# Kernel tuning notes

Hardware: AMD Instinct MI355X
Metric: run time of the kernel (lower is better)

## Reference

```python
import jax, jax.numpy as jnp
import numpy as np

N_PAPER = 100000
N_AUTHOR = 50000
E = 800000
D_IN, D_HID, D_OUT = 128, 128, 64


def seg_max(x, src, dst, num_segments):
    # adj_t.matmul(x, reduce='max'): per-destination max over neighbor features;
    # destinations with no in-edges get 0 (torch_sparse convention).
    m = jax.ops.segment_max(x[src], dst, num_segments=num_segments)
    return jnp.where(jnp.isneginf(m), jnp.zeros((), m.dtype), m)


def setup_inputs() -> dict:
    key = jax.random.key(0)
    ks = jax.random.split(key, 32)
    inp = {}
    inp['x_paper'] = jax.random.normal(ks[0], (N_PAPER, D_IN), jnp.float32)
    inp['emb_author'] = jax.random.normal(ks[1], (N_AUTHOR, D_IN), jnp.float32)
    inp['writes_src'] = jax.random.randint(ks[2], (E,), 0, N_AUTHOR, jnp.int32)
    inp['writes_dst'] = jax.random.randint(ks[3], (E,), 0, N_PAPER, jnp.int32)
    inp['cites_src'] = jax.random.randint(ks[4], (E,), 0, N_PAPER, jnp.int32)
    inp['cites_dst'] = jax.random.randint(ks[5], (E,), 0, N_PAPER, jnp.int32)
    inp['wb_src'] = jax.random.randint(ks[6], (E,), 0, N_PAPER, jnp.int32)
    inp['wb_dst'] = jax.random.randint(ks[7], (E,), 0, N_AUTHOR, jnp.int32)

    def lin_w(k, din, dout):
        s = 1.0 / np.sqrt(din)
        return jax.random.uniform(k, (din, dout), jnp.float32, -s, s)

    # layer 1: D_IN -> D_HID
    inp['w1_rel_writes'] = lin_w(ks[8], D_IN, D_HID)
    inp['w1_rel_cites'] = lin_w(ks[9], D_IN, D_HID)
    inp['w1_rel_wb'] = lin_w(ks[10], D_IN, D_HID)
    inp['w1_root_paper'] = lin_w(ks[11], D_IN, D_HID)
    inp['b1_root_paper'] = jnp.zeros((D_HID,), jnp.float32)
    inp['w1_root_author'] = lin_w(ks[12], D_IN, D_HID)
    inp['b1_root_author'] = jnp.zeros((D_HID,), jnp.float32)
    # layer 2: D_HID -> D_OUT
    inp['w2_rel_writes'] = lin_w(ks[13], D_HID, D_OUT)
    inp['w2_rel_cites'] = lin_w(ks[14], D_HID, D_OUT)
    inp['w2_rel_wb'] = lin_w(ks[15], D_HID, D_OUT)
    inp['w2_root_paper'] = lin_w(ks[16], D_HID, D_OUT)
    inp['b2_root_paper'] = jnp.zeros((D_OUT,), jnp.float32)
    inp['w2_root_author'] = lin_w(ks[17], D_HID, D_OUT)
    inp['b2_root_author'] = jnp.zeros((D_OUT,), jnp.float32)
    return inp


def _conv(xp, xa, edges, w_writes, w_cites, w_wb, w_rp, b_rp, w_ra, b_ra):
    writes_src, writes_dst, cites_src, cites_dst, wb_src, wb_dst = edges
    out_p = xp @ w_rp + b_rp
    out_a = xa @ w_ra + b_ra
    out_p = out_p + seg_max(xa, writes_src, writes_dst, N_PAPER) @ w_writes
    out_p = out_p + seg_max(xp, cites_src, cites_dst, N_PAPER) @ w_cites
    out_a = out_a + seg_max(xp, wb_src, wb_dst, N_AUTHOR) @ w_wb
    return out_p, out_a


def reference(x_paper, emb_author,
              writes_src, writes_dst, cites_src, cites_dst, wb_src, wb_dst,
              w1_rel_writes, w1_rel_cites, w1_rel_wb,
              w1_root_paper, b1_root_paper, w1_root_author, b1_root_author,
              w2_rel_writes, w2_rel_cites, w2_rel_wb,
              w2_root_paper, b2_root_paper, w2_root_author, b2_root_author):
    edges = (writes_src, writes_dst, cites_src, cites_dst, wb_src, wb_dst)
    hp, ha = _conv(x_paper, emb_author, edges,
                   w1_rel_writes, w1_rel_cites, w1_rel_wb,
                   w1_root_paper, b1_root_paper, w1_root_author, b1_root_author)
    hp, ha = jax.nn.relu(hp), jax.nn.relu(ha)  # dropout p=0 -> identity
    return _conv(hp, ha, edges,
                 w2_rel_writes, w2_rel_cites, w2_rel_wb,
                 w2_root_paper, b2_root_paper, w2_root_author, b2_root_author)
```

## Files before the change

kernel.cpp:

```cpp
#include <hip/hip_runtime.h>


#define DI 128
#define NP 100000
#define NA 50000
#define EPB 4096
#define MAXBIN 391

typedef short s8v __attribute__((ext_vector_type(8)));
typedef float f32x4 __attribute__((ext_vector_type(4)));

__device__ __forceinline__ unsigned short bf16_rne(float f) {
  unsigned int fb = __float_as_uint(f);
  fb += 0x7FFFu + ((fb >> 16) & 1u);
  return (unsigned short)(fb >> 16);
}

struct R3Args {
  const int* src[3]; const int* dst[3];
  int* bh[3]; int* bhs[3];
  unsigned int* tmp[3];
  int* bkt[3]; int* cnt[3]; int* rs[3];
  int E[3]; int N[3]; int nbin[3]; int NB[3];
};

__global__ __launch_bounds__(256) void radix_s1_k(R3Args a) {
  int y = blockIdx.y, blk = blockIdx.x;
  int NB = a.NB[y];
  if (blk >= NB) return;
  __shared__ int hist[MAXBIN];
  int nbin = a.nbin[y];
  for (int i = threadIdx.x; i < nbin; i += 256) hist[i] = 0;
  __syncthreads();
  int e0 = blk * EPB, e1 = min(e0 + EPB, a.E[y]);
  const int* dst = a.dst[y];
  for (int e = e0 + threadIdx.x; e < e1; e += 256)
    atomicAdd(&hist[dst[e] >> 8], 1);
  __syncthreads();
  int* bh = a.bh[y];
  for (int i = threadIdx.x; i < nbin; i += 256) bh[i * NB + blk] = hist[i];
}

__global__ __launch_bounds__(256) void radix_x1_k(R3Args a) {
  int y = blockIdx.y, blk = blockIdx.x;
  int NB = a.NB[y];
  if (blk >= NB) return;
  __shared__ int cur[MAXBIN];
  int nbin = a.nbin[y];
  const int* bhs = a.bhs[y];
  for (int i = threadIdx.x; i < nbin; i += 256) cur[i] = bhs[i * NB + blk];
  __syncthreads();
  int e0 = blk * EPB, e1 = min(e0 + EPB, a.E[y]);
  const int* dst = a.dst[y];
  const int* src = a.src[y];
  unsigned int* tmp = a.tmp[y];
  for (int e = e0 + threadIdx.x; e < e1; e += 256) {
    int d = dst[e];
    int pos = atomicAdd(&cur[d >> 8], 1);
    tmp[pos] = ((unsigned int)(d & 255) << 24) | (unsigned int)src[e];
  }
}

struct WArgs {
  const float* w[10];
  unsigned short* wf[10];
};

struct P2CArgs {
  R3Args ra;
  WArgs wa;
  const float* Xp; unsigned short* Yp; int n4p;
  const float* Xa; unsigned short* Ya; int n4a;
  int p2Blocks;
  int maxbin;
};

__global__ __launch_bounds__(256) void p2cvt_k(P2CArgs a) {
  int bid = blockIdx.x;
  int t = threadIdx.x;
  if (bid < a.p2Blocks) {
    int y = bid / a.maxbin, bin = bid % a.maxbin;
    if (bin >= a.ra.nbin[y]) return;
    __shared__ int hist[256], scn[256], cursor[256];
    hist[t] = 0;
    __syncthreads();
    const int* bhs = a.ra.bhs[y];
    int NB = a.ra.NB[y];
    int base = bhs[bin * NB];
    int end  = (bin + 1 < a.ra.nbin[y]) ? bhs[(bin + 1) * NB] : a.ra.E[y];
    const unsigned int* tmp = a.ra.tmp[y];
    for (int i = base + t; i < end; i += 256)
      atomicAdd(&hist[tmp[i] >> 24], 1);
    __syncthreads();
    int v = hist[t];
    scn[t] = v; __syncthreads();
    int acc = v;
    for (int o = 1; o < 256; o <<= 1) {
      int u = (t >= o) ? scn[t - o] : 0;
      __syncthreads();
      acc += u; scn[t] = acc;
      __syncthreads();
    }
    int ex = acc - v;
    cursor[t] = ex;
    int d = bin * 256 + t;
    if (d < a.ra.N[y]) { a.ra.cnt[y][d] = v; a.ra.rs[y][d] = base + ex; }
    __syncthreads();
    int* bkt = a.ra.bkt[y];
    for (int i = base + t; i < end; i += 256) {
      unsigned int p = tmp[i];
      int pos = atomicAdd(&cursor[p >> 24], 1);
      bkt[base + pos] = (int)((p & 0xFFFFFFu) << 8);
    }
    return;
  }
  bid -= a.p2Blocks;
  if (bid < 80) {
    int widx = bid >> 3;
    int OUTi = (widx < 5) ? 128 : 64;
    int CF = OUTi / 16;
    int nt = 4 * CF * 64;
    int tg = (bid & 7) * 256 + t;
    if (tg >= nt) return;
    int lane = tg & 63, tmp2 = tg >> 6;
    int cf = tmp2 % CF, kc = tmp2 / CF;
    int k0 = kc * 32 + (lane >> 4) * 8;
    int c  = cf * 16 + (lane & 15);
    const float* w = a.wa.w[widx];
    s8v v;
    #pragma unroll
    for (int i = 0; i < 8; ++i) v[i] = (short)bf16_rne(w[(k0 + i) * OUTi + c]);
    *(reinterpret_cast<s8v*>(a.wa.wf[widx]) + tg) = v;
    return;
  }
  bid -= 80;
  int i = bid * 256 + t;
  const float* X; unsigned short* Y;
  if (i < a.n4p) { X = a.Xp; Y = a.Yp; }
  else { i -= a.n4p; if (i >= a.n4a) return; X = a.Xa; Y = a.Ya; }
  float4 f = reinterpret_cast<const float4*>(X)[i];
  ushort4 o;
  o.x = bf16_rne(f.x); o.y = bf16_rne(f.y); o.z = bf16_rne(f.z); o.w = bf16_rne(f.w);
  reinterpret_cast<ushort4*>(Y)[i] = o;
}

struct S3Args {
  const int* cnt[3]; int* bsum[3]; int* rs[3];
  int n[3]; int nb[3];
};

__global__ __launch_bounds__(256) void blocksum3_k(S3Args a) {
  int y = blockIdx.y;
  int n = a.n[y];
  if (blockIdx.x * 1024 >= n) return;
  __shared__ int red[256];
  int t = threadIdx.x;
  int base = blockIdx.x * 1024 + t * 4;
  int s = 0;
  #pragma unroll
  for (int i = 0; i < 4; ++i) { int idx = base + i; if (idx < n) s += a.cnt[y][idx]; }
  red[t] = s; __syncthreads();
  #pragma unroll
  for (int o = 128; o > 0; o >>= 1) { if (t < o) red[t] += red[t + o]; __syncthreads(); }
  if (t == 0) a.bsum[y][blockIdx.x] = red[0];
}

__global__ __launch_bounds__(256) void partials3_k(S3Args a) {
  __shared__ int sm[256];
  int y = blockIdx.x;
  int nb = a.nb[y];
  int t = threadIdx.x;
  int v = (t < nb) ? a.bsum[y][t] : 0;
  sm[t] = v; __syncthreads();
  int acc = v;
  for (int o = 1; o < 256; o <<= 1) {
    int u = (t >= o) ? sm[t - o] : 0;
    __syncthreads();
    acc += u; sm[t] = acc;
    __syncthreads();
  }
  if (t < nb) a.bsum[y][t] = acc - v;
}

__global__ __launch_bounds__(256) void scanwrite3_k(S3Args a) {
  int y = blockIdx.y;
  int n = a.n[y];
  if (blockIdx.x * 1024 >= n) return;
  __shared__ int ts[256];
  int t = threadIdx.x;
  int base = blockIdx.x * 1024 + t * 4;
  int v[4]; int s = 0;
  #pragma unroll
  for (int i = 0; i < 4; ++i) { int idx = base + i; v[i] = (idx < n) ? a.cnt[y][idx] : 0; s += v[i]; }
  ts[t] = s; __syncthreads();
  int inc = s;
  for (int o = 1; o < 256; o <<= 1) {
    int u = (t >= o) ? ts[t - o] : 0;
    __syncthreads();
    inc += u; ts[t] = inc;
    __syncthreads();
  }
  int p = a.bsum[y][blockIdx.x] + inc - s;
  #pragma unroll
  for (int i = 0; i < 4; ++i) { int idx = base + i; if (idx < n) { a.rs[y][idx] = p; p += v[i]; } }
}

struct G3Args {
  const int* cnt[3]; const int* rs[3]; const int* bkt[3];
  const unsigned short* X[3]; unsigned short* S[3];
  int N[3];
};

__global__ __launch_bounds__(256) void gather3_k(G3Args a) {
  const int y = blockIdx.y;
  const int lane = threadIdx.x & 63;
  const int wave = threadIdx.x >> 6;
  const int g = lane >> 4, lg = lane & 15;
  const int d = blockIdx.x * 16 + wave * 4 + g;
  if (d >= a.N[y]) return;

  unsigned short* So = a.S[y] + (size_t)d * DI + lg * 8;
  const int deg = a.cnt[y][d];
  if (deg == 0) {
    uint4 z; z.x = z.y = z.z = z.w = 0u;
    *reinterpret_cast<uint4*>(So) = z;
    return;
  }
  const int* bp = a.bkt[y] + a.rs[y][d];
  const char* Xb = reinterpret_cast<const char*>(a.X[y]) + lg * 16;

  float ml[4], mh[4];
  #pragma unroll
  for (int j = 0; j < 4; ++j) { ml[j] = -3.4e38f; mh[j] = -3.4e38f; }

  int s0 = bp[0];
  for (int e = 0; e < deg; e += 4) {
    int s1 = (e + 1 < deg) ? bp[e + 1] : s0;
    int s2 = (e + 2 < deg) ? bp[e + 2] : s0;
    int s3 = (e + 3 < deg) ? bp[e + 3] : s0;
    int sn = (e + 4 < deg) ? bp[e + 4] : s0;
    uint4 r0 = *reinterpret_cast<const uint4*>(Xb + s0);
    uint4 r1 = *reinterpret_cast<const uint4*>(Xb + s1);
    uint4 r2 = *reinterpret_cast<const uint4*>(Xb + s2);
    uint4 r3 = *reinterpret_cast<const uint4*>(Xb + s3);
    unsigned int w0[4] = {r0.x, r0.y, r0.z, r0.w};
    unsigned int w1[4] = {r1.x, r1.y, r1.z, r1.w};
    unsigned int w2[4] = {r2.x, r2.y, r2.z, r2.w};
    unsigned int w3[4] = {r3.x, r3.y, r3.z, r3.w};
    #pragma unroll
    for (int j = 0; j < 4; ++j) {
      float tl = fmaxf(fmaxf(__uint_as_float(w0[j] << 16), __uint_as_float(w1[j] << 16)),
                       __uint_as_float(w2[j] << 16));
      ml[j] = fmaxf(fmaxf(ml[j], __uint_as_float(w3[j] << 16)), tl);
      float th = fmaxf(fmaxf(__uint_as_float(w0[j]), __uint_as_float(w1[j])),
                       __uint_as_float(w2[j]));
      mh[j] = fmaxf(fmaxf(mh[j], __uint_as_float(w3[j])), th);
    }
    s0 = sn;
  }
  uint4 o;
  o.x = (__float_as_uint(ml[0]) >> 16) | (__float_as_uint(mh[0]) & 0xFFFF0000u);
  o.y = (__float_as_uint(ml[1]) >> 16) | (__float_as_uint(mh[1]) & 0xFFFF0000u);
  o.z = (__float_as_uint(ml[2]) >> 16) | (__float_as_uint(mh[2]) & 0xFFFF0000u);
  o.w = (__float_as_uint(ml[3]) >> 16) | (__float_as_uint(mh[3]) & 0xFFFF0000u);
  *reinterpret_cast<uint4*>(So) = o;
}

template<int CF>
__device__ __forceinline__ void mfma_accum(const unsigned short* __restrict__ A,
                                           const unsigned short* __restrict__ W,
                                           f32x4* acc, size_t arow, int lane, int half) {
  const s8v* a = reinterpret_cast<const s8v*>(A + arow * DI + half * 8);
  const s8v* w = reinterpret_cast<const s8v*>(W) + lane;
  #pragma unroll
  for (int kc = 0; kc < 4; ++kc) {
    s8v av = a[kc * 4];
    #pragma unroll
    for (int cf = 0; cf < CF; ++cf)
      acc[cf] = __builtin_amdgcn_mfma_f32_16x16x32_bf16(av, w[(kc * CF + cf) * 64], acc[cf], 0, 0, 0);
  }
}

struct GemmPairArgs {
  const unsigned short *A0[2], *W0[2], *A1[2], *W1[2], *A2, *W2;
  const float* bias[2];
  void* out[2];
  int N[2];
  int blocks0;
};

template<int OUT, bool RELU, bool OUT_BF16>
__global__ __launch_bounds__(256) void gemm_pair_k(GemmPairArgs g) {
  constexpr int CF = OUT / 16;
  const int p = (blockIdx.x >= (unsigned)g.blocks0) ? 1 : 0;
  const int brow = blockIdx.x - (p ? g.blocks0 : 0);
  const int N = g.N[p];
  const int lane = threadIdx.x & 63;
  const int wave = threadIdx.x >> 6;
  const int row0 = brow * 64 + wave * 16;
  if (row0 >= N) return;
  const int rl = lane & 15, half = lane >> 4;
  const size_t arow = (size_t)(row0 + rl);

  f32x4 acc[CF];
  #pragma unroll
  for (int i = 0; i < CF; ++i) acc[i] = f32x4{0.f, 0.f, 0.f, 0.f};

  mfma_accum<CF>(g.A0[p], g.W0[p], acc, arow, lane, half);
  mfma_accum<CF>(g.A1[p], g.W1[p], acc, arow, lane, half);
  if (!p) mfma_accum<CF>(g.A2, g.W2, acc, arow, lane, half);

  const float* bias = g.bias[p];
  #pragma unroll
  for (int cf = 0; cf < CF; ++cf) {
    float bv = bias[cf * 16 + rl];
    #pragma unroll
    for (int j = 0; j < 4; ++j) {
      int r = row0 + half * 4 + j;
      if (r >= N) continue;
      float v = acc[cf][j] + bv;
      if (RELU) v = v > 0.f ? v : 0.f;
      size_t idx = (size_t)r * OUT + cf * 16 + rl;
      if (OUT_BF16) ((unsigned short*)g.out[p])[idx] = bf16_rne(v);
      else          __builtin_nontemporal_store(v, (float*)g.out[p] + idx);
    }
  }
}

extern "C" void kernel_launch(void* const* d_in, const int* in_sizes, int n_in,
                              void* d_out, int out_size, void* d_ws, size_t ws_size,
                              hipStream_t stream) {
  const float* xp = (const float*)d_in[0];
  const float* xa = (const float*)d_in[1];
  const int* wsrc = (const int*)d_in[2];
  const int* wdst = (const int*)d_in[3];
  const int* csrc = (const int*)d_in[4];
  const int* cdst = (const int*)d_in[5];
  const int* bsrc = (const int*)d_in[6];
  const int* bdst = (const int*)d_in[7];
  const int Ew = in_sizes[2], Ec = in_sizes[4], Eb = in_sizes[6];

  const float* w1w  = (const float*)d_in[8];
  const float* w1c  = (const float*)d_in[9];
  const float* w1wb = (const float*)d_in[10];
  const float* w1rp = (const float*)d_in[11];
  const float* b1rp = (const float*)d_in[12];
  const float* w1ra = (const float*)d_in[13];
  const float* b1ra = (const float*)d_in[14];
  const float* w2w  = (const float*)d_in[15];
  const float* w2c  = (const float*)d_in[16];
  const float* w2wb = (const float*)d_in[17];
  const float* w2rp = (const float*)d_in[18];
  const float* b2rp = (const float*)d_in[19];
  const float* w2ra = (const float*)d_in[20];
  const float* b2ra = (const float*)d_in[21];

  char* ws = (char*)d_ws;
  unsigned short* xpb = (unsigned short*)(ws + 0);
  unsigned short* xab = (unsigned short*)(ws + 25600000);
  unsigned short* hp  = (unsigned short*)(ws + 38400000);
  unsigned short* ha  = (unsigned short*)(ws + 64000000);
  unsigned short* S_w = (unsigned short*)(ws + 76800000);
  unsigned short* S_c = (unsigned short*)(ws + 102400000);
  unsigned short* S_b = (unsigned short*)(ws + 128000000);
  int* bkt_w = (int*)(ws + 140800000);
  int* bkt_c = (int*)(ws + 144000000);
  int* bkt_b = (int*)(ws + 147200000);
  int* cnt_w = (int*)(ws + 150400000);
  int* cnt_c = (int*)(ws + 150800000);
  int* cnt_b = (int*)(ws + 151200000);
  int* rs_w  = (int*)(ws + 151400000);
  int* rs_c  = (int*)(ws + 151800000);
  int* rs_b  = (int*)(ws + 152200000);
  int* bsum_w = (int*)(ws + 152400000);
  int* bsum_c = (int*)(ws + 152404096);
  int* bsum_b = (int*)(ws + 152408192);
  unsigned short* wf = (unsigned short*)(ws + 152412288);
  unsigned int* tmp_w = (unsigned int*)(ws + 152660000);
  unsigned int* tmp_c = (unsigned int*)(ws + 155860000);
  unsigned int* tmp_b = (unsigned int*)(ws + 159060000);
  int* bh_w  = (int*)(ws + 76800000);
  int* bh_c  = (int*)(ws + 77110000);
  int* bh_b  = (int*)(ws + 77420000);
  int* bhs_w = (int*)(ws + 77580000);
  int* bhs_c = (int*)(ws + 77890000);
  int* bhs_b = (int*)(ws + 78200000);

  unsigned short* WF[10];
  size_t off = 0;
  for (int i = 0; i < 10; ++i) {
    WF[i] = wf + off;
    off += (i < 5) ? (size_t)128 * 128 : (size_t)128 * 64;
  }

  float* outP = (float*)d_out;
  float* outA = outP + (size_t)NP * 64;

  const int gP = (NP + 63) / 64, gA = (NA + 63) / 64;
  const int gG = (NP + 15) / 16;

  R3Args ra;
  ra.src[0] = wsrc; ra.dst[0] = wdst; ra.E[0] = Ew; ra.N[0] = NP;
  ra.src[1] = csrc; ra.dst[1] = cdst; ra.E[1] = Ec; ra.N[1] = NP;
  ra.src[2] = bsrc; ra.dst[2] = bdst; ra.E[2] = Eb; ra.N[2] = NA;
  ra.bh[0] = bh_w; ra.bh[1] = bh_c; ra.bh[2] = bh_b;
  ra.bhs[0] = bhs_w; ra.bhs[1] = bhs_c; ra.bhs[2] = bhs_b;
  ra.tmp[0] = tmp_w; ra.tmp[1] = tmp_c; ra.tmp[2] = tmp_b;
  ra.bkt[0] = bkt_w; ra.bkt[1] = bkt_c; ra.bkt[2] = bkt_b;
  ra.cnt[0] = cnt_w; ra.cnt[1] = cnt_c; ra.cnt[2] = cnt_b;
  ra.rs[0] = rs_w; ra.rs[1] = rs_c; ra.rs[2] = rs_b;
  int gSX = 0, gSC = 0, maxbin = 0;
  for (int y = 0; y < 3; ++y) {
    ra.nbin[y] = (ra.N[y] + 255) >> 8;
    ra.NB[y] = (ra.E[y] + EPB - 1) / EPB;
    if (ra.NB[y] > gSX) gSX = ra.NB[y];
    if (ra.nbin[y] > maxbin) maxbin = ra.nbin[y];
  }
  S3Args sa;
  sa.bsum[0] = bsum_w; sa.bsum[1] = bsum_c; sa.bsum[2] = bsum_b;
  for (int y = 0; y < 3; ++y) {
    sa.cnt[y] = ra.bh[y]; sa.rs[y] = ra.bhs[y];
    sa.n[y] = ra.nbin[y] * ra.NB[y];
    sa.nb[y] = (sa.n[y] + 1023) / 1024;
    if (sa.nb[y] > gSC) gSC = sa.nb[y];
  }

  const int n4p = NP * DI / 4, n4a = NA * DI / 4;
  P2CArgs pc;
  pc.ra = ra;
  const float* wsrcs[10] = {w1w, w1c, w1wb, w1rp, w1ra, w2w, w2c, w2wb, w2rp, w2ra};
  for (int i = 0; i < 10; ++i) { pc.wa.w[i] = wsrcs[i]; pc.wa.wf[i] = WF[i]; }
  pc.Xp = xp; pc.Yp = xpb; pc.n4p = n4p;
  pc.Xa = xa; pc.Ya = xab; pc.n4a = n4a;
  pc.maxbin = maxbin;
  pc.p2Blocks = 3 * maxbin;
  const int gPC = pc.p2Blocks + 80 + (n4p + n4a + 255) / 256;

  G3Args g1, g2;
  for (int i = 0; i < 3; ++i) {
    g1.cnt[i] = g2.cnt[i] = (i == 0) ? cnt_w : (i == 1) ? cnt_c : cnt_b;
    g1.rs[i]  = g2.rs[i]  = (i == 0) ? rs_w  : (i == 1) ? rs_c  : rs_b;
    g1.bkt[i] = g2.bkt[i] = (i == 0) ? bkt_w : (i == 1) ? bkt_c : bkt_b;
    g1.S[i]   = g2.S[i]   = (i == 0) ? S_w   : (i == 1) ? S_c   : S_b;
    g1.N[i]   = g2.N[i]   = (i == 2) ? NA : NP;
  }
  g1.X[0] = xab; g1.X[1] = xpb; g1.X[2] = xpb;
  g2.X[0] = ha;  g2.X[1] = hp;  g2.X[2] = hp;

  GemmPairArgs p1, p2;
  p1.A0[0] = xpb; p1.W0[0] = WF[3]; p1.A1[0] = S_w; p1.W1[0] = WF[0]; p1.A2 = S_c; p1.W2 = WF[1];
  p1.bias[0] = b1rp; p1.out[0] = hp; p1.N[0] = NP;
  p1.A0[1] = xab; p1.W0[1] = WF[4]; p1.A1[1] = S_b; p1.W1[1] = WF[2];
  p1.bias[1] = b1ra; p1.out[1] = ha; p1.N[1] = NA;
  p1.blocks0 = gP;
  p2.A0[0] = hp; p2.W0[0] = WF[8]; p2.A1[0] = S_w; p2.W1[0] = WF[5]; p2.A2 = S_c; p2.W2 = WF[6];
  p2.bias[0] = b2rp; p2.out[0] = outP; p2.N[0] = NP;
  p2.A0[1] = ha; p2.W0[1] = WF[9]; p2.A1[1] = S_b; p2.W1[1] = WF[7];
  p2.bias[1] = b2ra; p2.out[1] = outA; p2.N[1] = NA;
  p2.blocks0 = gP;

  radix_s1_k<<<dim3(gSX, 3), 256, 0, stream>>>(ra);
  blocksum3_k<<<dim3(gSC, 3), 256, 0, stream>>>(sa);
  partials3_k<<<3, 256, 0, stream>>>(sa);
  scanwrite3_k<<<dim3(gSC, 3), 256, 0, stream>>>(sa);
  radix_x1_k<<<dim3(gSX, 3), 256, 0, stream>>>(ra);
  p2cvt_k<<<gPC, 256, 0, stream>>>(pc);

  gather3_k<<<dim3(gG, 3), 256, 0, stream>>>(g1);
  gemm_pair_k<128, true, true><<<gP + gA, 256, 0, stream>>>(p1);

  gather3_k<<<dim3(gG, 3), 256, 0, stream>>>(g2);
  gemm_pair_k<64, false, false><<<gP + gA, 256, 0, stream>>>(p2);
}
```

Measured before the change: 334.5 us.

## Fuse CSR build stages into one cooperative kernel with grid syncs

Measured after the change: 936.3 us. +179.9%, slower.

```diff
diff --git a/kernel.cpp b/kernel.cpp
--- a/kernel.cpp
+++ b/kernel.cpp
@@ -1,4 +1,7 @@
 #include <hip/hip_runtime.h>
+#include <hip/hip_cooperative_groups.h>
+
+namespace cg = cooperative_groups;
 
 
 #define DI 128
@@ -23,186 +26,214 @@
   int* bkt[3]; int* cnt[3]; int* rs[3];
   int E[3]; int N[3]; int nbin[3]; int NB[3];
 };
-
-__global__ __launch_bounds__(256) void radix_s1_k(R3Args a) {
-  int y = blockIdx.y, blk = blockIdx.x;
-  int NB = a.NB[y];
-  if (blk >= NB) return;
-  __shared__ int hist[MAXBIN];
-  int nbin = a.nbin[y];
-  for (int i = threadIdx.x; i < nbin; i += 256) hist[i] = 0;
-  __syncthreads();
-  int e0 = blk * EPB, e1 = min(e0 + EPB, a.E[y]);
-  const int* dst = a.dst[y];
-  for (int e = e0 + threadIdx.x; e < e1; e += 256)
-    atomicAdd(&hist[dst[e] >> 8], 1);
-  __syncthreads();
-  int* bh = a.bh[y];
-  for (int i = threadIdx.x; i < nbin; i += 256) bh[i * NB + blk] = hist[i];
-}
-
-__global__ __launch_bounds__(256) void radix_x1_k(R3Args a) {
-  int y = blockIdx.y, blk = blockIdx.x;
-  int NB = a.NB[y];
-  if (blk >= NB) return;
-  __shared__ int cur[MAXBIN];
-  int nbin = a.nbin[y];
-  const int* bhs = a.bhs[y];
-  for (int i = threadIdx.x; i < nbin; i += 256) cur[i] = bhs[i * NB + blk];
-  __syncthreads();
-  int e0 = blk * EPB, e1 = min(e0 + EPB, a.E[y]);
-  const int* dst = a.dst[y];
-  const int* src = a.src[y];
-  unsigned int* tmp = a.tmp[y];
-  for (int e = e0 + threadIdx.x; e < e1; e += 256) {
-    int d = dst[e];
-    int pos = atomicAdd(&cur[d >> 8], 1);
-    tmp[pos] = ((unsigned int)(d & 255) << 24) | (unsigned int)src[e];
-  }
-}
-
+struct S3Args {
+  const int* cnt[3]; int* bsum[3]; int* rs[3];
+  int n[3]; int nb[3];
+};
 struct WArgs {
   const float* w[10];
   unsigned short* wf[10];
 };
-
-struct P2CArgs {
+struct CoopArgs {
   R3Args ra;
+  S3Args sa;
   WArgs wa;
   const float* Xp; unsigned short* Yp; int n4p;
   const float* Xa; unsigned short* Ya; int n4a;
-  int p2Blocks;
-  int maxbin;
+  int maxNB, maxnb, maxbin;
+  int nCvt;
 };
 
-__global__ __launch_bounds__(256) void p2cvt_k(P2CArgs a) {
-  int bid = blockIdx.x;
-  int t = threadIdx.x;
-  if (bid < a.p2Blocks) {
-    int y = bid / a.maxbin, bin = bid % a.maxbin;
-    if (bin >= a.ra.nbin[y]) return;
-    __shared__ int hist[256], scn[256], cursor[256];
-    hist[t] = 0;
-    __syncthreads();
-    const int* bhs = a.ra.bhs[y];
-    int NB = a.ra.NB[y];
-    int base = bhs[bin * NB];
-    int end  = (bin + 1 < a.ra.nbin[y]) ? bhs[(bin + 1) * NB] : a.ra.E[y];
-    const unsigned int* tmp = a.ra.tmp[y];
-    for (int i = base + t; i < end; i += 256)
-      atomicAdd(&hist[tmp[i] >> 24], 1);
-    __syncthreads();
-    int v = hist[t];
-    scn[t] = v; __syncthreads();
-    int acc = v;
-    for (int o = 1; o < 256; o <<= 1) {
-      int u = (t >= o) ? scn[t - o] : 0;
+__global__ __launch_bounds__(256) void coop_csr_k(CoopArgs a) {
+  cg::grid_group grid = cg::this_grid();
+  __shared__ int lds[768];
+  const int t = threadIdx.x;
+  const int GB = gridDim.x;
+
+  {
+    const int vb_s1 = 3 * a.maxNB;
+    const int vbTot = vb_s1 + 80 + a.nCvt;
+    for (int vb = blockIdx.x; vb < vbTot; vb += GB) {
+      if (vb < vb_s1) {
+        int y = vb / a.maxNB, blk = vb % a.maxNB;
+        int NB = a.ra.NB[y];
+        if (blk < NB) {
+          int nbin = a.ra.nbin[y];
+          for (int i = t; i < nbin; i += 256) lds[i] = 0;
+          __syncthreads();
+          int e0 = blk * EPB, e1 = min(e0 + EPB, a.ra.E[y]);
+          const int* dst = a.ra.dst[y];
+          for (int e = e0 + t; e < e1; e += 256) atomicAdd(&lds[dst[e] >> 8], 1);
+          __syncthreads();
+          int* bh = a.ra.bh[y];
+          for (int i = t; i < nbin; i += 256) bh[i * NB + blk] = lds[i];
+          __syncthreads();
+        }
+      } else if (vb < vb_s1 + 80) {
+        int b = vb - vb_s1;
+        int widx = b >> 3;
+        int OUTi = (widx < 5) ? 128 : 64;
+        int CF = OUTi / 16;
+        int nt = 4 * CF * 64;
+        int tg = (b & 7) * 256 + t;
+        if (tg < nt) {
+          int lane = tg & 63, tmp2 = tg >> 6;
+          int cf = tmp2 % CF, kc = tmp2 / CF;
+          int k0 = kc * 32 + (lane >> 4) * 8;
+          int c  = cf * 16 + (lane & 15);
+          const float* w = a.wa.w[widx];
+          s8v v;
+          #pragma unroll
+          for (int i = 0; i < 8; ++i) v[i] = (short)bf16_rne(w[(k0 + i) * OUTi + c]);
+          *(reinterpret_cast<s8v*>(a.wa.wf[widx]) + tg) = v;
+        }
+      } else {
+        int i = (vb - vb_s1 - 80) * 256 + t;
+        const float* X; unsigned short* Y;
+        bool ok = true;
+        if (i < a.n4p) { X = a.Xp; Y = a.Yp; }
+        else { i -= a.n4p; if (i >= a.n4a) ok = false; else { X = a.Xa; Y = a.Ya; } }
+        if (ok) {
+          float4 f = reinterpret_cast<const float4*>(X)[i];
+          ushort4 o;
+          o.x = bf16_rne(f.x); o.y = bf16_rne(f.y); o.z = bf16_rne(f.z); o.w = bf16_rne(f.w);
+          reinterpret_cast<ushort4*>(Y)[i] = o;
+        }
+      }
+    }
+  }
+  grid.sync();
+
+  {
+    const int vbTot = 3 * a.maxnb;
+    for (int vb = blockIdx.x; vb < vbTot; vb += GB) {
+      int y = vb / a.maxnb, blk = vb % a.maxnb;
+      int n = a.sa.n[y];
+      if (blk * 1024 < n) {
+        int base = blk * 1024 + t * 4;
+        int s = 0;
+        #pragma unroll
+        for (int i = 0; i < 4; ++i) { int idx = base + i; if (idx < n) s += a.sa.cnt[y][idx]; }
+        lds[t] = s; __syncthreads();
+        #pragma unroll
+        for (int o = 128; o > 0; o >>= 1) { if (t < o) lds[t] += lds[t + o]; __syncthreads(); }
+        if (t == 0) a.sa.bsum[y][blk] = lds[0];
+        __syncthreads();
+      }
+    }
+  }
+  grid.sync();
+
+  {
+    for (int vb = blockIdx.x; vb < 3; vb += GB) {
+      int nb = a.sa.nb[vb];
+      int v = (t < nb) ? a.sa.bsum[vb][t] : 0;
+      lds[t] = v; __syncthreads();
+      int acc = v;
+      for (int o = 1; o < 256; o <<= 1) {
+        int u = (t >= o) ? lds[t - o] : 0;
+        __syncthreads();
+        acc += u; lds[t] = acc;
+        __syncthreads();
+      }
+      if (t < nb) a.sa.bsum[vb][t] = acc - v;
       __syncthreads();
-      acc += u; scn[t] = acc;
-      __syncthreads();
-    }
-    int ex = acc - v;
-    cursor[t] = ex;
-    int d = bin * 256 + t;
-    if (d < a.ra.N[y]) { a.ra.cnt[y][d] = v; a.ra.rs[y][d] = base + ex; }
-    __syncthreads();
-    int* bkt = a.ra.bkt[y];
-    for (int i = base + t; i < end; i += 256) {
-      unsigned int p = tmp[i];
-      int pos = atomicAdd(&cursor[p >> 24], 1);
-      bkt[base + pos] = (int)((p & 0xFFFFFFu) << 8);
-    }
-    return;
-  }
-  bid -= a.p2Blocks;
-  if (bid < 80) {
-    int widx = bid >> 3;
-    int OUTi = (widx < 5) ? 128 : 64;
-    int CF = OUTi / 16;
-    int nt = 4 * CF * 64;
-    int tg = (bid & 7) * 256 + t;
-    if (tg >= nt) return;
-    int lane = tg & 63, tmp2 = tg >> 6;
-    int cf = tmp2 % CF, kc = tmp2 / CF;
-    int k0 = kc * 32 + (lane >> 4) * 8;
-    int c  = cf * 16 + (lane & 15);
-    const float* w = a.wa.w[widx];
-    s8v v;
-    #pragma unroll
-    for (int i = 0; i < 8; ++i) v[i] = (short)bf16_rne(w[(k0 + i) * OUTi + c]);
-    *(reinterpret_cast<s8v*>(a.wa.wf[widx]) + tg) = v;
-    return;
-  }
-  bid -= 80;
-  int i = bid * 256 + t;
-  const float* X; unsigned short* Y;
-  if (i < a.n4p) { X = a.Xp; Y = a.Yp; }
-  else { i -= a.n4p; if (i >= a.n4a) return; X = a.Xa; Y = a.Ya; }
-  float4 f = reinterpret_cast<const float4*>(X)[i];
-  ushort4 o;
-  o.x = bf16_rne(f.x); o.y = bf16_rne(f.y); o.z = bf16_rne(f.z); o.w = bf16_rne(f.w);
-  reinterpret_cast<ushort4*>(Y)[i] = o;
-}
-
-struct S3Args {
-  const int* cnt[3]; int* bsum[3]; int* rs[3];
-  int n[3]; int nb[3];
-};
-
-__global__ __launch_bounds__(256) void blocksum3_k(S3Args a) {
-  int y = blockIdx.y;
-  int n = a.n[y];
-  if (blockIdx.x * 1024 >= n) return;
-  __shared__ int red[256];
-  int t = threadIdx.x;
-  int base = blockIdx.x * 1024 + t * 4;
-  int s = 0;
-  #pragma unroll
-  for (int i = 0; i < 4; ++i) { int idx = base + i; if (idx < n) s += a.cnt[y][idx]; }
-  red[t] = s; __syncthreads();
-  #pragma unroll
-  for (int o = 128; o > 0; o >>= 1) { if (t < o) red[t] += red[t + o]; __syncthreads(); }
-  if (t == 0) a.bsum[y][blockIdx.x] = red[0];
-}
-
-__global__ __launch_bounds__(256) void partials3_k(S3Args a) {
-  __shared__ int sm[256];
-  int y = blockIdx.x;
-  int nb = a.nb[y];
-  int t = threadIdx.x;
-  int v = (t < nb) ? a.bsum[y][t] : 0;
-  sm[t] = v; __syncthreads();
-  int acc = v;
-  for (int o = 1; o < 256; o <<= 1) {
-    int u = (t >= o) ? sm[t - o] : 0;
-    __syncthreads();
-    acc += u; sm[t] = acc;
-    __syncthreads();
-  }
-  if (t < nb) a.bsum[y][t] = acc - v;
-}
-
-__global__ __launch_bounds__(256) void scanwrite3_k(S3Args a) {
-  int y = blockIdx.y;
-  int n = a.n[y];
-  if (blockIdx.x * 1024 >= n) return;
-  __shared__ int ts[256];
-  int t = threadIdx.x;
-  int base = blockIdx.x * 1024 + t * 4;
-  int v[4]; int s = 0;
-  #pragma unroll
-  for (int i = 0; i < 4; ++i) { int idx = base + i; v[i] = (idx < n) ? a.cnt[y][idx] : 0; s += v[i]; }
-  ts[t] = s; __syncthreads();
-  int inc = s;
-  for (int o = 1; o < 256; o <<= 1) {
-    int u = (t >= o) ? ts[t - o] : 0;
-    __syncthreads();
-    inc += u; ts[t] = inc;
-    __syncthreads();
-  }
-  int p = a.bsum[y][blockIdx.x] + inc - s;
-  #pragma unroll
-  for (int i = 0; i < 4; ++i) { int idx = base + i; if (idx < n) { a.rs[y][idx] = p; p += v[i]; } }
+    }
+  }
+  grid.sync();
+
+  {
+    const int vbTot = 3 * a.maxnb;
+    for (int vb = blockIdx.x; vb < vbTot; vb += GB) {
+      int y = vb / a.maxnb, blk = vb % a.maxnb;
+      int n = a.sa.n[y];
+      if (blk * 1024 < n) {
+        int base = blk * 1024 + t * 4;
+        int v[4]; int s = 0;
+        #pragma unroll
+        for (int i = 0; i < 4; ++i) { int idx = base + i; v[i] = (idx < n) ? a.sa.cnt[y][idx] : 0; s += v[i]; }
+        lds[t] = s; __syncthreads();
+        int inc = s;
+        for (int o = 1; o < 256; o <<= 1) {
+          int u = (t >= o) ? lds[t - o] : 0;
+          __syncthreads();
+          inc += u; lds[t] = inc;
+          __syncthreads();
+        }
+        int p = a.sa.bsum[y][blk] + inc - s;
+        #pragma unroll
+        for (int i = 0; i < 4; ++i) { int idx = base + i; if (idx < n) { a.sa.rs[y][idx] = p; p += v[i]; } }
+        __syncthreads();
+      }
+    }
+  }
+  grid.sync();
+
+  {
+    const int vbTot = 3 * a.maxNB;
+    for (int vb = blockIdx.x; vb < vbTot; vb += GB) {
+      int y = vb / a.maxNB, blk = vb % a.maxNB;
+      int NB = a.ra.NB[y];
+      if (blk < NB) {
+        int nbin = a.ra.nbin[y];
+        const int* bhs = a.ra.bhs[y];
+        for (int i = t; i < nbin; i += 256) lds[i] = bhs[i * NB + blk];
+        __syncthreads();
+        int e0 = blk * EPB, e1 = min(e0 + EPB, a.ra.E[y]);
+        const int* dst = a.ra.dst[y];
+        const int* src = a.ra.src[y];
+        unsigned int* tmp = a.ra.tmp[y];
+        for (int e = e0 + t; e < e1; e += 256) {
+          int d = dst[e];
+          int pos = atomicAdd(&lds[d >> 8], 1);
+          tmp[pos] = ((unsigned int)(d & 255) << 24) | (unsigned int)src[e];
+        }
+        __syncthreads();
+      }
+    }
+  }
+  grid.sync();
+
+  {
+    int* hist = lds; int* scn = lds + 256; int* cursor = lds + 512;
+    const int vbTot = 3 * a.maxbin;
+    for (int vb = blockIdx.x; vb < vbTot; vb += GB) {
+      int y = vb / a.maxbin, bin = vb % a.maxbin;
+      if (bin < a.ra.nbin[y]) {
+        hist[t] = 0;
+        __syncthreads();
+        const int* bhs = a.ra.bhs[y];
+        int NB = a.ra.NB[y];
+        int base = bhs[bin * NB];
+        int end  = (bin + 1 < a.ra.nbin[y]) ? bhs[(bin + 1) * NB] : a.ra.E[y];
+        const unsigned int* tmp = a.ra.tmp[y];
+        for (int i = base + t; i < end; i += 256)
+          atomicAdd(&hist[tmp[i] >> 24], 1);
+        __syncthreads();
+        int v = hist[t];
+        scn[t] = v; __syncthreads();
+        int acc = v;
+        for (int o = 1; o < 256; o <<= 1) {
+          int u = (t >= o) ? scn[t - o] : 0;
+          __syncthreads();
+          acc += u; scn[t] = acc;
+          __syncthreads();
+        }
+        int ex = acc - v;
+        cursor[t] = ex;
+        int d = bin * 256 + t;
+        if (d < a.ra.N[y]) { a.ra.cnt[y][d] = v; a.ra.rs[y][d] = base + ex; }
+        __syncthreads();
+        int* bkt = a.ra.bkt[y];
+        for (int i = base + t; i < end; i += 256) {
+          unsigned int p = tmp[i];
+          int pos = atomicAdd(&cursor[p >> 24], 1);
+          bkt[base + pos] = (int)((p & 0xFFFFFFu) << 8);
+        }
+        __syncthreads();
+      }
+    }
+  }
 }
 
 struct G3Args {
@@ -409,11 +440,11 @@
   ra.bkt[0] = bkt_w; ra.bkt[1] = bkt_c; ra.bkt[2] = bkt_b;
   ra.cnt[0] = cnt_w; ra.cnt[1] = cnt_c; ra.cnt[2] = cnt_b;
   ra.rs[0] = rs_w; ra.rs[1] = rs_c; ra.rs[2] = rs_b;
-  int gSX = 0, gSC = 0, maxbin = 0;
+  int maxNB = 0, maxnb = 0, maxbin = 0;
   for (int y = 0; y < 3; ++y) {
     ra.nbin[y] = (ra.N[y] + 255) >> 8;
     ra.NB[y] = (ra.E[y] + EPB - 1) / EPB;
-    if (ra.NB[y] > gSX) gSX = ra.NB[y];
+    if (ra.NB[y] > maxNB) maxNB = ra.NB[y];
     if (ra.nbin[y] > maxbin) maxbin = ra.nbin[y];
   }
   S3Args sa;
@@ -422,19 +453,19 @@
     sa.cnt[y] = ra.bh[y]; sa.rs[y] = ra.bhs[y];
     sa.n[y] = ra.nbin[y] * ra.NB[y];
     sa.nb[y] = (sa.n[y] + 1023) / 1024;
-    if (sa.nb[y] > gSC) gSC = sa.nb[y];
+    if (sa.nb[y] > maxnb) maxnb = sa.nb[y];
   }
 
   const int n4p = NP * DI / 4, n4a = NA * DI / 4;
-  P2CArgs pc;
-  pc.ra = ra;
+  CoopArgs ca;
+  ca.ra = ra;
+  ca.sa = sa;
   const float* wsrcs[10] = {w1w, w1c, w1wb, w1rp, w1ra, w2w, w2c, w2wb, w2rp, w2ra};
-  for (int i = 0; i < 10; ++i) { pc.wa.w[i] = wsrcs[i]; pc.wa.wf[i] = WF[i]; }
-  pc.Xp = xp; pc.Yp = xpb; pc.n4p = n4p;
-  pc.Xa = xa; pc.Ya = xab; pc.n4a = n4a;
-  pc.maxbin = maxbin;
-  pc.p2Blocks = 3 * maxbin;
-  const int gPC = pc.p2Blocks + 80 + (n4p + n4a + 255) / 256;
+  for (int i = 0; i < 10; ++i) { ca.wa.w[i] = wsrcs[i]; ca.wa.wf[i] = WF[i]; }
+  ca.Xp = xp; ca.Yp = xpb; ca.n4p = n4p;
+  ca.Xa = xa; ca.Ya = xab; ca.n4a = n4a;
+  ca.maxNB = maxNB; ca.maxnb = maxnb; ca.maxbin = maxbin;
+  ca.nCvt = (n4p + n4a + 255) / 256;
 
   G3Args g1, g2;
   for (int i = 0; i < 3; ++i) {
@@ -459,12 +490,11 @@
   p2.bias[1] = b2ra; p2.out[1] = outA; p2.N[1] = NA;
   p2.blocks0 = gP;
 
-  radix_s1_k<<<dim3(gSX, 3), 256, 0, stream>>>(ra);
-  blocksum3_k<<<dim3(gSC, 3), 256, 0, stream>>>(sa);
-  partials3_k<<<3, 256, 0, stream>>>(sa);
-  scanwrite3_k<<<dim3(gSC, 3), 256, 0, stream>>>(sa);
-  radix_x1_k<<<dim3(gSX, 3), 256, 0, stream>>>(ra);
-  p2cvt_k<<<gPC, 256, 0, stream>>>(pc);
+  {
+    void* kargs[] = { (void*)&ca };
+    hipLaunchCooperativeKernel((void*)coop_csr_k, dim3(1024), dim3(256),
+                               kargs, 0, stream);
+  }
 
   gather3_k<<<dim3(gG, 3), 256, 0, stream>>>(g1);
   gemm_pair_k<128, true, true><<<gP + gA, 256, 0, stream>>>(p1);
```

## Replace three-kernel bin scan with single-block scan and larger edge chunks

Applied to the files above, without the earlier changes.

Result: slower. 377.7 us (+12.9%).

```diff
diff --git a/kernel.cpp b/kernel.cpp
--- a/kernel.cpp
+++ b/kernel.cpp
@@ -4,7 +4,7 @@
 #define DI 128
 #define NP 100000
 #define NA 50000
-#define EPB 4096
+#define EPB 16384
 #define MAXBIN 391
 
 typedef short s8v __attribute__((ext_vector_type(8)));
@@ -58,6 +58,42 @@
     int d = dst[e];
     int pos = atomicAdd(&cur[d >> 8], 1);
     tmp[pos] = ((unsigned int)(d & 255) << 24) | (unsigned int)src[e];
+  }
+}
+
+struct S1Args {
+  const int* cnt[3]; int* rs[3];
+  int n[3];
+};
+
+__global__ __launch_bounds__(1024) void scan1_k(S1Args a) {
+  const int y = blockIdx.x;
+  const int n = a.n[y];
+  const int t = threadIdx.x;
+  __shared__ int sm[1024];
+  __shared__ int carryS;
+  if (t == 0) carryS = 0;
+  __syncthreads();
+  for (int base = 0; base < n; base += 4096) {
+    int idx = base + t * 4;
+    int v[4]; int s = 0;
+    #pragma unroll
+    for (int i = 0; i < 4; ++i) { int k = idx + i; v[i] = (k < n) ? a.cnt[y][k] : 0; s += v[i]; }
+    sm[t] = s; __syncthreads();
+    int acc = s;
+    for (int o = 1; o < 1024; o <<= 1) {
+      int u = (t >= o) ? sm[t - o] : 0;
+      __syncthreads();
+      acc += u; sm[t] = acc;
+      __syncthreads();
+    }
+    int carry = carryS;
+    int p = carry + acc - s;
+    #pragma unroll
+    for (int i = 0; i < 4; ++i) { int k = idx + i; if (k < n) { a.rs[y][k] = p; p += v[i]; } }
+    __syncthreads();
+    if (t == 1023) carryS = carry + acc;
+    __syncthreads();
   }
 }
 
@@ -144,67 +180,6 @@
   reinterpret_cast<ushort4*>(Y)[i] = o;
 }
 
-struct S3Args {
-  const int* cnt[3]; int* bsum[3]; int* rs[3];
-  int n[3]; int nb[3];
-};
-
-__global__ __launch_bounds__(256) void blocksum3_k(S3Args a) {
-  int y = blockIdx.y;
-  int n = a.n[y];
-  if (blockIdx.x * 1024 >= n) return;
-  __shared__ int red[256];
-  int t = threadIdx.x;
-  int base = blockIdx.x * 1024 + t * 4;
-  int s = 0;
-  #pragma unroll
-  for (int i = 0; i < 4; ++i) { int idx = base + i; if (idx < n) s += a.cnt[y][idx]; }
-  red[t] = s; __syncthreads();
-  #pragma unroll
-  for (int o = 128; o > 0; o >>= 1) { if (t < o) red[t] += red[t + o]; __syncthreads(); }
-  if (t == 0) a.bsum[y][blockIdx.x] = red[0];
-}
-
-__global__ __launch_bounds__(256) void partials3_k(S3Args a) {
-  __shared__ int sm[256];
-  int y = blockIdx.x;
-  int nb = a.nb[y];
-  int t = threadIdx.x;
-  int v = (t < nb) ? a.bsum[y][t] : 0;
-  sm[t] = v; __syncthreads();
-  int acc = v;
-  for (int o = 1; o < 256; o <<= 1) {
-    int u = (t >= o) ? sm[t - o] : 0;
-    __syncthreads();
-    acc += u; sm[t] = acc;
-    __syncthreads();
-  }
-  if (t < nb) a.bsum[y][t] = acc - v;
-}
-
-__global__ __launch_bounds__(256) void scanwrite3_k(S3Args a) {
-  int y = blockIdx.y;
-  int n = a.n[y];
-  if (blockIdx.x * 1024 >= n) return;
-  __shared__ int ts[256];
-  int t = threadIdx.x;
-  int base = blockIdx.x * 1024 + t * 4;
-  int v[4]; int s = 0;
-  #pragma unroll
-  for (int i = 0; i < 4; ++i) { int idx = base + i; v[i] = (idx < n) ? a.cnt[y][idx] : 0; s += v[i]; }
-  ts[t] = s; __syncthreads();
-  int inc = s;
-  for (int o = 1; o < 256; o <<= 1) {
-    int u = (t >= o) ? ts[t - o] : 0;
-    __syncthreads();
-    inc += u; ts[t] = inc;
-    __syncthreads();
-  }
-  int p = a.bsum[y][blockIdx.x] + inc - s;
-  #pragma unroll
-  for (int i = 0; i < 4; ++i) { int idx = base + i; if (idx < n) { a.rs[y][idx] = p; p += v[i]; } }
-}
-
 struct G3Args {
   const int* cnt[3]; const int* rs[3]; const int* bkt[3];
   const unsigned short* X[3]; unsigned short* S[3];
@@ -372,9 +347,6 @@
   int* rs_w  = (int*)(ws + 151400000);
   int* rs_c  = (int*)(ws + 151800000);
   int* rs_b  = (int*)(ws + 152200000);
-  int* bsum_w = (int*)(ws + 152400000);
-  int* bsum_c = (int*)(ws + 152404096);
-  int* bsum_b = (int*)(ws + 152408192);
   unsigned short* wf = (unsigned short*)(ws + 152412288);
   unsigned int* tmp_w = (unsigned int*)(ws + 152660000);
   unsigned int* tmp_c = (unsigned int*)(ws + 155860000);
@@ -409,20 +381,17 @@
   ra.bkt[0] = bkt_w; ra.bkt[1] = bkt_c; ra.bkt[2] = bkt_b;
   ra.cnt[0] = cnt_w; ra.cnt[1] = cnt_c; ra.cnt[2] = cnt_b;
   ra.rs[0] = rs_w; ra.rs[1] = rs_c; ra.rs[2] = rs_b;
-  int gSX = 0, gSC = 0, maxbin = 0;
+  int gSX = 0, maxbin = 0;
   for (int y = 0; y < 3; ++y) {
     ra.nbin[y] = (ra.N[y] + 255) >> 8;
     ra.NB[y] = (ra.E[y] + EPB - 1) / EPB;
     if (ra.NB[y] > gSX) gSX = ra.NB[y];
     if (ra.nbin[y] > maxbin) maxbin = ra.nbin[y];
   }
-  S3Args sa;
-  sa.bsum[0] = bsum_w; sa.bsum[1] = bsum_c; sa.bsum[2] = bsum_b;
+  S1Args sc;
   for (int y = 0; y < 3; ++y) {
-    sa.cnt[y] = ra.bh[y]; sa.rs[y] = ra.bhs[y];
-    sa.n[y] = ra.nbin[y] * ra.NB[y];
-    sa.nb[y] = (sa.n[y] + 1023) / 1024;
-    if (sa.nb[y] > gSC) gSC = sa.nb[y];
+    sc.cnt[y] = ra.bh[y]; sc.rs[y] = ra.bhs[y];
+    sc.n[y] = ra.nbin[y] * ra.NB[y];
   }
 
   const int n4p = NP * DI / 4, n4a = NA * DI / 4;
@@ -460,9 +429,7 @@
   p2.blocks0 = gP;
 
   radix_s1_k<<<dim3(gSX, 3), 256, 0, stream>>>(ra);
-  blocksum3_k<<<dim3(gSC, 3), 256, 0, stream>>>(sa);
-  partials3_k<<<3, 256, 0, stream>>>(sa);
-  scanwrite3_k<<<dim3(gSC, 3), 256, 0, stream>>>(sa);
+  scan1_k<<<3, 1024, 0, stream>>>(sc);
   radix_x1_k<<<dim3(gSX, 3), 256, 0, stream>>>(ra);
   p2cvt_k<<<gPC, 256, 0, stream>>>(pc);
 
```
